# Kernel optimization log

Measured on AMD Instinct MI355X. Metric: run time of the kernel, lower is better.

Reference implementation:

```python
import jax, jax.numpy as jnp
import numpy as np

N, H = 8192, 1024

def setup_inputs() -> dict:
    key = jax.random.key(0)
    ks = jax.random.split(key, 7)
    s = 1.0 / np.sqrt(H)
    return {
        "x": jax.random.normal(ks[0], (N, H), dtype=jnp.float32),
        "Wq": jax.random.uniform(ks[1], (H, H), dtype=jnp.float32, minval=-s, maxval=s),
        "bq": jax.random.uniform(ks[2], (H,), dtype=jnp.float32, minval=-s, maxval=s),
        "Wk": jax.random.uniform(ks[3], (H, H), dtype=jnp.float32, minval=-s, maxval=s),
        "bk": jax.random.uniform(ks[4], (H,), dtype=jnp.float32, minval=-s, maxval=s),
        "Wv": jax.random.uniform(ks[5], (H, H), dtype=jnp.float32, minval=-s, maxval=s),
        "bv": jax.random.uniform(ks[6], (H,), dtype=jnp.float32, minval=-s, maxval=s),
    }

def reference(x, Wq, bq, Wk, bk, Wv, bv):
    # q/k/v projections: [N, H]
    q = x @ Wq + bq
    k = x @ Wk + bk
    v = x @ Wv + bv
    # full scores [N, N]; NOTE: original has no 1/sqrt(d) scaling
    scores = q @ k.T
    alpha = jax.nn.softmax(scores, axis=1)
    return alpha @ v
```

## Files before the change

kernel.cpp:

```cpp
#include <hip/hip_runtime.h>
#include <hip/hip_bf16.h>
#include <hip/hip_fp16.h>


typedef _Float16 f16x8 __attribute__((ext_vector_type(8)));
typedef float floatx4 __attribute__((ext_vector_type(4)));

__device__ __forceinline__ unsigned short f2h(float f) {
  __half h = __float2half(f);
  return __builtin_bit_cast(unsigned short, h);
}

__device__ __forceinline__ void async16(const void* g, void* l) {
  __builtin_amdgcn_global_load_lds(
      (__attribute__((address_space(1))) unsigned int*)(g),
      (__attribute__((address_space(3))) unsigned int*)(l),
      16, 0, 0);
}


__global__ __launch_bounds__(256) void conv_f32_f16(const float* __restrict__ in,
                                                    unsigned short* __restrict__ out,
                                                    long n) {
  long i = ((long)blockIdx.x * 256 + threadIdx.x) * 4;
  if (i + 3 < n) {
    float4 f = *(const float4*)(in + i);
    ushort4 o;
    o.x = f2h(f.x); o.y = f2h(f.y); o.z = f2h(f.z); o.w = f2h(f.w);
    *(ushort4*)(out + i) = o;
  }
}

__global__ __launch_bounds__(256) void transpose_f32_f16_3(const float* __restrict__ in0,
                                                           const float* __restrict__ in1,
                                                           const float* __restrict__ in2,
                                                           unsigned short* __restrict__ out,
                                                           int rows, int cols) {
  const float* in = (blockIdx.z == 0) ? in0 : (blockIdx.z == 1) ? in1 : in2;
  unsigned short* o = out + (size_t)blockIdx.z * rows * cols;
  __shared__ float tile[32][33];
  int bx = blockIdx.x * 32;
  int by = blockIdx.y * 32;
  int tx = threadIdx.x & 31, ty = threadIdx.x >> 5;
  #pragma unroll
  for (int yy = ty; yy < 32; yy += 8)
    tile[yy][tx] = in[(size_t)(by + yy) * cols + bx + tx];
  __syncthreads();
  #pragma unroll
  for (int yy = ty; yy < 32; yy += 8)
    o[(size_t)(bx + yy) * rows + by + tx] = f2h(tile[tx][yy]);
}

__global__ __launch_bounds__(256) void transpose_u16(const unsigned short* __restrict__ in,
                                                     unsigned short* __restrict__ out,
                                                     int rows, int cols) {
  __shared__ unsigned short tile[32][33];
  int bx = blockIdx.x * 32;
  int by = blockIdx.y * 32;
  int tx = threadIdx.x & 31, ty = threadIdx.x >> 5;
  #pragma unroll
  for (int yy = ty; yy < 32; yy += 8)
    tile[yy][tx] = in[(size_t)(by + yy) * cols + bx + tx];
  __syncthreads();
  #pragma unroll
  for (int yy = ty; yy < 32; yy += 8)
    out[(size_t)(bx + yy) * rows + by + tx] = tile[tx][yy];
}

template <int MODE>
__global__ __launch_bounds__(256, 4)
void gemm_bt(const unsigned short* __restrict__ A,
             const unsigned short* __restrict__ B,
             int M, int Nn, int K,
             const float* __restrict__ b0, const float* __restrict__ b1,
             const float* __restrict__ b2,
             unsigned short* __restrict__ out) {
  if constexpr (MODE == 0) {
    B   += (size_t)blockIdx.z * Nn * K;
    out += (size_t)blockIdx.z * M * Nn;
  }
  const float* bias = (MODE != 0) ? nullptr
                      : (blockIdx.z == 0) ? b0 : (blockIdx.z == 1) ? b1 : b2;
  __shared__ unsigned short As[128 * 32];
  __shared__ unsigned short Bs[128 * 32];
  const int tid  = threadIdx.x;
  const int wave = tid >> 6;
  const int lane = tid & 63;
  const int wm = wave >> 1, wn = wave & 1;
  const int quad = lane >> 4, l16 = lane & 15;
  const long bm = (long)blockIdx.y * 128;
  const long bn = (long)blockIdx.x * 128;

  floatx4 acc[4][4] = {};

  const int srow = wave * 32 + (lane >> 2);
  const int scol = (lane & 3) * 8;
  const unsigned short* gA0 = A + (bm + srow) * (long)K + scol;
  const unsigned short* gA1 = gA0 + 16L * K;
  const unsigned short* gB0 = B + (bn + srow) * (long)K + scol;
  const unsigned short* gB1 = gB0 + 16L * K;
  unsigned short* lA0 = &As[(wave * 32) * 32];
  unsigned short* lA1 = &As[(wave * 32 + 16) * 32];
  unsigned short* lB0 = &Bs[(wave * 32) * 32];
  unsigned short* lB1 = &Bs[(wave * 32 + 16) * 32];

  for (int kk = 0; kk < K; kk += 32) {
    async16(gA0 + kk, lA0);
    async16(gA1 + kk, lA1);
    async16(gB0 + kk, lB0);
    async16(gB1 + kk, lB1);
    __syncthreads();
    f16x8 af[4], bfv[4];
    #pragma unroll
    for (int i = 0; i < 4; ++i) {
      af[i]  = *reinterpret_cast<const f16x8*>(&As[(wm * 64 + i * 16 + l16) * 32 + quad * 8]);
      bfv[i] = *reinterpret_cast<const f16x8*>(&Bs[(wn * 64 + i * 16 + l16) * 32 + quad * 8]);
    }
    #pragma unroll
    for (int i = 0; i < 4; ++i)
      #pragma unroll
      for (int j = 0; j < 4; ++j)
        acc[i][j] = __builtin_amdgcn_mfma_f32_16x16x32_f16(af[i], bfv[j], acc[i][j], 0, 0, 0);
    __syncthreads();
  }

  #pragma unroll
  for (int i = 0; i < 4; ++i) {
    const long row0 = bm + wm * 64 + i * 16 + quad * 4;
    #pragma unroll
    for (int j = 0; j < 4; ++j) {
      const long col = bn + wn * 64 + j * 16 + l16;
      float badd = (MODE == 0) ? bias[col] : 0.0f;
      #pragma unroll
      for (int r = 0; r < 4; ++r)
        out[(row0 + r) * (long)Nn + col] = f2h(acc[i][j][r] + badd);
    }
  }
}

__global__ __launch_bounds__(512, 4)
void gemm_pv(const unsigned short* __restrict__ A,
             const unsigned short* __restrict__ B,
             int M, int Nn, int K, int kchunk,
             float* __restrict__ out) {
  __shared__ unsigned short As[128 * 32];
  __shared__ unsigned short Bs[256 * 32];
  const int tid  = threadIdx.x;
  const int wave = tid >> 6;
  const int lane = tid & 63;
  const int wm = wave >> 2;
  const int wn = wave & 3;
  const int quad = lane >> 4, l16 = lane & 15;
  const long bm = (long)blockIdx.y * 128;
  const long bn = (long)blockIdx.x * 256;
  const int kbase = blockIdx.z * kchunk;

  floatx4 acc[4][4] = {};

  const int scol = (lane & 3) * 8;
  const unsigned short* gA  = A + (bm + wave * 16 + (lane >> 2)) * (long)K + scol + kbase;
  const unsigned short* gB0 = B + (bn + wave * 32 + (lane >> 2)) * (long)K + scol + kbase;
  const unsigned short* gB1 = gB0 + 16L * K;
  unsigned short* lA  = &As[(wave * 16) * 32];
  unsigned short* lB0 = &Bs[(wave * 32) * 32];
  unsigned short* lB1 = &Bs[(wave * 32 + 16) * 32];

  for (int kk = 0; kk < kchunk; kk += 32) {
    async16(gA + kk, lA);
    async16(gB0 + kk, lB0);
    async16(gB1 + kk, lB1);
    __syncthreads();
    f16x8 af[4], bfv[4];
    #pragma unroll
    for (int i = 0; i < 4; ++i) {
      af[i]  = *reinterpret_cast<const f16x8*>(&As[(wm * 64 + i * 16 + l16) * 32 + quad * 8]);
      bfv[i] = *reinterpret_cast<const f16x8*>(&Bs[(wn * 64 + i * 16 + l16) * 32 + quad * 8]);
    }
    #pragma unroll
    for (int i = 0; i < 4; ++i)
      #pragma unroll
      for (int j = 0; j < 4; ++j)
        acc[i][j] = __builtin_amdgcn_mfma_f32_16x16x32_f16(af[i], bfv[j], acc[i][j], 0, 0, 0);
    __syncthreads();
  }

  #pragma unroll
  for (int i = 0; i < 4; ++i) {
    const long row0 = bm + wm * 64 + i * 16 + quad * 4;
    #pragma unroll
    for (int j = 0; j < 4; ++j) {
      const long col = bn + wn * 64 + j * 16 + l16;
      #pragma unroll
      for (int r = 0; r < 4; ++r)
        atomicAdd(&out[(row0 + r) * (long)Nn + col], acc[i][j][r]);
    }
  }
}

__global__ __launch_bounds__(256) void softmax_rows(unsigned short* __restrict__ S, int n) {
  const int row = blockIdx.x;
  const int tid = threadIdx.x;
  const int lane = tid & 63, w = tid >> 6;
  unsigned short* prow = S + (size_t)row * n;
  const __half* hrow = (const __half*)prow;

  float v[32];
  float m = -1e30f;
  #pragma unroll
  for (int i = 0; i < 32; ++i) {
    v[i] = __half2float(hrow[i * 256 + tid]);
    m = fmaxf(m, v[i]);
  }
  #pragma unroll
  for (int off = 32; off > 0; off >>= 1) m = fmaxf(m, __shfl_down(m, off, 64));
  __shared__ float redm[4];
  if (lane == 0) redm[w] = m;
  __syncthreads();
  m = fmaxf(fmaxf(redm[0], redm[1]), fmaxf(redm[2], redm[3]));

  float s = 0.0f;
  #pragma unroll
  for (int i = 0; i < 32; ++i) {
    v[i] = __expf(v[i] - m);
    s += v[i];
  }
  #pragma unroll
  for (int off = 32; off > 0; off >>= 1) s += __shfl_down(s, off, 64);
  __shared__ float reds[4];
  if (lane == 0) reds[w] = s;
  __syncthreads();
  s = reds[0] + reds[1] + reds[2] + reds[3];
  const float inv = 1.0f / s;

  #pragma unroll
  for (int i = 0; i < 32; ++i) prow[i * 256 + tid] = f2h(v[i] * inv);
}

extern "C" void kernel_launch(void* const* d_in, const int* in_sizes, int n_in,
                              void* d_out, int out_size, void* d_ws, size_t ws_size,
                              hipStream_t stream) {
  const int N = 8192, H = 1024;
  const float* x  = (const float*)d_in[0];
  const float* Wq = (const float*)d_in[1];
  const float* bq = (const float*)d_in[2];
  const float* Wk = (const float*)d_in[3];
  const float* bk = (const float*)d_in[4];
  const float* Wv = (const float*)d_in[5];
  const float* bv = (const float*)d_in[6];

  char* p = (char*)d_ws;
  unsigned short* xh  = (unsigned short*)p; p += (size_t)N * H * 2;
  unsigned short* WT  = (unsigned short*)p; p += (size_t)3 * H * H * 2;
  unsigned short* qkv = (unsigned short*)p; p += (size_t)3 * N * H * 2;
  unsigned short* vth = (unsigned short*)p; p += (size_t)N * H * 2;
  unsigned short* S   = (unsigned short*)p; p += (size_t)N * N * 2;
  if ((size_t)(p - (char*)d_ws) > ws_size) return;
  unsigned short* qh = qkv;
  unsigned short* kh = qkv + (size_t)N * H;
  unsigned short* vh = qkv + (size_t)2 * N * H;

  conv_f32_f16<<<(N * H / 4 + 255) / 256, 256, 0, stream>>>(x, xh, (long)N * H);
  transpose_f32_f16_3<<<dim3(H / 32, H / 32, 3), 256, 0, stream>>>(Wq, Wk, Wv, WT, H, H);

  gemm_bt<0><<<dim3(H / 128, N / 128, 3), 256, 0, stream>>>(xh, WT, N, H, H, bq, bk, bv, qkv);
  transpose_u16<<<dim3(H / 32, N / 32), 256, 0, stream>>>(vh, vth, N, H);

  gemm_bt<1><<<dim3(N / 128, N / 128), 256, 0, stream>>>(qh, kh, N, N, H,
                                                         nullptr, nullptr, nullptr, S);
  softmax_rows<<<N, 256, 0, stream>>>(S, N);

  hipMemsetAsync(d_out, 0, (size_t)N * H * 4, stream);
  gemm_pv<<<dim3(H / 256, N / 128, 2), 512, 0, stream>>>(S, vth, N, H, N, N / 2,
                                                         (float*)d_out);
}
```

Measured before the change: 601.8 us.

## Compute V transposed directly, widen PV k-tile with swizzled LDS, split-K by four

V^T is now produced directly by a GEMM of Wv^T against x with a per-row bias, which drops the separate V projection output and its transpose kernel. The PV GEMM loads 64-wide K tiles with an XOR swizzle to avoid LDS bank conflicts and runs two MFMA sub-steps per barrier, halving the number of syncs. Split-K goes from 2 to 4 to put more blocks in flight. The cost is more fp32 atomics on the output and twice the LDS per block.

```diff
diff --git a/kernel.cpp b/kernel.cpp
--- a/kernel.cpp
+++ b/kernel.cpp
@@ -51,36 +51,20 @@
     o[(size_t)(bx + yy) * rows + by + tx] = f2h(tile[tx][yy]);
 }
 
-__global__ __launch_bounds__(256) void transpose_u16(const unsigned short* __restrict__ in,
-                                                     unsigned short* __restrict__ out,
-                                                     int rows, int cols) {
-  __shared__ unsigned short tile[32][33];
-  int bx = blockIdx.x * 32;
-  int by = blockIdx.y * 32;
-  int tx = threadIdx.x & 31, ty = threadIdx.x >> 5;
-  #pragma unroll
-  for (int yy = ty; yy < 32; yy += 8)
-    tile[yy][tx] = in[(size_t)(by + yy) * cols + bx + tx];
-  __syncthreads();
-  #pragma unroll
-  for (int yy = ty; yy < 32; yy += 8)
-    out[(size_t)(bx + yy) * rows + by + tx] = tile[tx][yy];
-}
-
 template <int MODE>
 __global__ __launch_bounds__(256, 4)
 void gemm_bt(const unsigned short* __restrict__ A,
              const unsigned short* __restrict__ B,
              int M, int Nn, int K,
              const float* __restrict__ b0, const float* __restrict__ b1,
-             const float* __restrict__ b2,
              unsigned short* __restrict__ out) {
   if constexpr (MODE == 0) {
     B   += (size_t)blockIdx.z * Nn * K;
     out += (size_t)blockIdx.z * M * Nn;
   }
-  const float* bias = (MODE != 0) ? nullptr
-                      : (blockIdx.z == 0) ? b0 : (blockIdx.z == 1) ? b1 : b2;
+  const float* bias = (MODE == 1) ? nullptr
+                      : (MODE == 2) ? b0
+                      : (blockIdx.z == 0) ? b0 : b1;
   __shared__ unsigned short As[128 * 32];
   __shared__ unsigned short Bs[128 * 32];
   const int tid  = threadIdx.x;
@@ -130,10 +114,13 @@
     #pragma unroll
     for (int j = 0; j < 4; ++j) {
       const long col = bn + wn * 64 + j * 16 + l16;
-      float badd = (MODE == 0) ? bias[col] : 0.0f;
-      #pragma unroll
-      for (int r = 0; r < 4; ++r)
-        out[(row0 + r) * (long)Nn + col] = f2h(acc[i][j][r] + badd);
+      const float cb = (MODE == 0) ? bias[col] : 0.0f;
+      #pragma unroll
+      for (int r = 0; r < 4; ++r) {
+        float v = acc[i][j][r] + cb;
+        if constexpr (MODE == 2) v += bias[row0 + r];
+        out[(row0 + r) * (long)Nn + col] = f2h(v);
+      }
     }
   }
 }
@@ -143,44 +130,54 @@
              const unsigned short* __restrict__ B,
              int M, int Nn, int K, int kchunk,
              float* __restrict__ out) {
-  __shared__ unsigned short As[128 * 32];
-  __shared__ unsigned short Bs[256 * 32];
+  __shared__ unsigned short As[128 * 64];
+  __shared__ unsigned short Bs[256 * 64];
   const int tid  = threadIdx.x;
   const int wave = tid >> 6;
+  const int wv   = __builtin_amdgcn_readfirstlane(wave);
   const int lane = tid & 63;
-  const int wm = wave >> 2;
-  const int wn = wave & 3;
+  const int wm = wv >> 2;
+  const int wn = wv & 3;
   const int quad = lane >> 4, l16 = lane & 15;
   const long bm = (long)blockIdx.y * 128;
   const long bn = (long)blockIdx.x * 256;
-  const int kbase = blockIdx.z * kchunk;
+  const long kbase = (long)blockIdx.z * kchunk;
 
   floatx4 acc[4][4] = {};
 
-  const int scol = (lane & 3) * 8;
-  const unsigned short* gA  = A + (bm + wave * 16 + (lane >> 2)) * (long)K + scol + kbase;
-  const unsigned short* gB0 = B + (bn + wave * 32 + (lane >> 2)) * (long)K + scol + kbase;
-  const unsigned short* gB1 = gB0 + 16L * K;
-  unsigned short* lA  = &As[(wave * 16) * 32];
-  unsigned short* lB0 = &Bs[(wave * 32) * 32];
-  unsigned short* lB1 = &Bs[(wave * 32 + 16) * 32];
-
-  for (int kk = 0; kk < kchunk; kk += 32) {
-    async16(gA + kk, lA);
-    async16(gB0 + kk, lB0);
-    async16(gB1 + kk, lB1);
-    __syncthreads();
-    f16x8 af[4], bfv[4];
-    #pragma unroll
-    for (int i = 0; i < 4; ++i) {
-      af[i]  = *reinterpret_cast<const f16x8*>(&As[(wm * 64 + i * 16 + l16) * 32 + quad * 8]);
-      bfv[i] = *reinterpret_cast<const f16x8*>(&Bs[(wn * 64 + i * 16 + l16) * 32 + quad * 8]);
-    }
-    #pragma unroll
-    for (int i = 0; i < 4; ++i)
-      #pragma unroll
-      for (int j = 0; j < 4; ++j)
-        acc[i][j] = __builtin_amdgcn_mfma_f32_16x16x32_f16(af[i], bfv[j], acc[i][j], 0, 0, 0);
+  const int rl = lane >> 3;
+  const int gc = (lane & 7) ^ rl;
+  const unsigned short* gA = A + (bm + rl) * (long)K + gc * 8 + kbase;
+  const unsigned short* gB = B + (bn + rl) * (long)K + gc * 8 + kbase;
+  const long opA0 = (long)(wv * 2) * 8 * K, opA1 = opA0 + 8L * K;
+  const long opB0 = (long)(wv * 4) * 8 * K, opB1 = opB0 + 8L * K;
+  const long opB2 = opB1 + 8L * K,          opB3 = opB2 + 8L * K;
+  unsigned short* lA = &As[(wv * 2) * 512];
+  unsigned short* lB = &Bs[(wv * 4) * 512];
+
+  for (int kk = 0; kk < kchunk; kk += 64) {
+    async16(gA + opA0 + kk, lA);
+    async16(gA + opA1 + kk, lA + 512);
+    async16(gB + opB0 + kk, lB);
+    async16(gB + opB1 + kk, lB + 512);
+    async16(gB + opB2 + kk, lB + 1024);
+    async16(gB + opB3 + kk, lB + 1536);
+    __syncthreads();
+    #pragma unroll
+    for (int ks = 0; ks < 2; ++ks) {
+      f16x8 af[4], bfv[4];
+      #pragma unroll
+      for (int i = 0; i < 4; ++i) {
+        const int ga = (ks * 4 + quad) ^ (l16 & 7);
+        af[i]  = *reinterpret_cast<const f16x8*>(&As[(wm * 64 + i * 16 + l16) * 64 + ga * 8]);
+        bfv[i] = *reinterpret_cast<const f16x8*>(&Bs[(wn * 64 + i * 16 + l16) * 64 + ga * 8]);
+      }
+      #pragma unroll
+      for (int i = 0; i < 4; ++i)
+        #pragma unroll
+        for (int j = 0; j < 4; ++j)
+          acc[i][j] = __builtin_amdgcn_mfma_f32_16x16x32_f16(af[i], bfv[j], acc[i][j], 0, 0, 0);
+    }
     __syncthreads();
   }
 
@@ -251,25 +248,25 @@
   char* p = (char*)d_ws;
   unsigned short* xh  = (unsigned short*)p; p += (size_t)N * H * 2;
   unsigned short* WT  = (unsigned short*)p; p += (size_t)3 * H * H * 2;
-  unsigned short* qkv = (unsigned short*)p; p += (size_t)3 * N * H * 2;
+  unsigned short* qk  = (unsigned short*)p; p += (size_t)2 * N * H * 2;
   unsigned short* vth = (unsigned short*)p; p += (size_t)N * H * 2;
   unsigned short* S   = (unsigned short*)p; p += (size_t)N * N * 2;
   if ((size_t)(p - (char*)d_ws) > ws_size) return;
-  unsigned short* qh = qkv;
-  unsigned short* kh = qkv + (size_t)N * H;
-  unsigned short* vh = qkv + (size_t)2 * N * H;
+  unsigned short* qh  = qk;
+  unsigned short* kh  = qk + (size_t)N * H;
+  unsigned short* WvT = WT + (size_t)2 * H * H;
 
   conv_f32_f16<<<(N * H / 4 + 255) / 256, 256, 0, stream>>>(x, xh, (long)N * H);
   transpose_f32_f16_3<<<dim3(H / 32, H / 32, 3), 256, 0, stream>>>(Wq, Wk, Wv, WT, H, H);
 
-  gemm_bt<0><<<dim3(H / 128, N / 128, 3), 256, 0, stream>>>(xh, WT, N, H, H, bq, bk, bv, qkv);
-  transpose_u16<<<dim3(H / 32, N / 32), 256, 0, stream>>>(vh, vth, N, H);
+  gemm_bt<0><<<dim3(H / 128, N / 128, 2), 256, 0, stream>>>(xh, WT, N, H, H, bq, bk, qk);
+  gemm_bt<2><<<dim3(N / 128, H / 128), 256, 0, stream>>>(WvT, xh, H, N, H, bv, nullptr, vth);
 
   gemm_bt<1><<<dim3(N / 128, N / 128), 256, 0, stream>>>(qh, kh, N, N, H,
-                                                         nullptr, nullptr, nullptr, S);
+                                                         nullptr, nullptr, S);
   softmax_rows<<<N, 256, 0, stream>>>(S, N);
 
   hipMemsetAsync(d_out, 0, (size_t)N * H * 4, stream);
-  gemm_pv<<<dim3(H / 256, N / 128, 2), 512, 0, stream>>>(S, vth, N, H, N, N / 2,
+  gemm_pv<<<dim3(H / 256, N / 128, 4), 512, 0, stream>>>(S, vth, N, H, N, N / 4,
                                                          (float*)d_out);
 }
```

Measured after the change: 591.6 us. About the same (-1.7%).
